# Kernel tuning notes

Measured on AMD Instinct MI355X. Metric: run time of the kernel, lower is better.

## Reference

```python
import jax, jax.numpy as jnp
import numpy as np

B, P, N, M = 8, 50, 128, 128          # batch, pomo, query nodes, route tokens
EMB, H, D = 128, 8, 16                # embedding_dim, head_num, qkv_dim
NE, K = 8, 2                          # num_experts, top-k
CLIP = 10.0                           # logit_clipping


def setup_inputs() -> dict:
    key = jax.random.key(0)
    ks = jax.random.split(key, 12)
    s = 0.02
    return {
        "encoded_nodes": jax.random.normal(ks[0], (B, P, N, EMB), jnp.float32),
        "encoded_routes": jax.random.normal(ks[1], (B, P, M, EMB + 1), jnp.float32),
        "ninf_mask": jnp.zeros((B, P, N), jnp.float32),
        "route_mask": jnp.zeros((B, P, N, M), jnp.float32),
        "Wq": s * jax.random.normal(ks[2], (EMB, H * D), jnp.float32),
        "Wk": s * jax.random.normal(ks[3], (EMB + 1, H * D), jnp.float32),
        "Wv": s * jax.random.normal(ks[4], (EMB + 1, H * D), jnp.float32),
        "Wg": s * jax.random.normal(ks[5], (H * D, NE), jnp.float32),
        "We": s * jax.random.normal(ks[6], (NE, H * D, EMB + 1), jnp.float32),
        "be": jnp.zeros((NE, EMB + 1), jnp.float32),
        "Wfinal": s * jax.random.normal(ks[7], (EMB + 1, 1), jnp.float32),
    }


def _heads(x, W):
    # x: [B,P,n,F] @ W[F,H*D] -> [B,P,H,n,D]
    y = x @ W
    b, p, n, _ = y.shape
    return jnp.swapaxes(y.reshape(b, p, n, H, D), 2, 3)


def reference(encoded_nodes, encoded_routes, ninf_mask, route_mask,
              Wq, Wk, Wv, Wg, We, be, Wfinal):
    # --- masked multi-head attention (multi_head_attention1) ---
    q = _heads(encoded_nodes, Wq)          # [B,P,H,N,D]
    k = _heads(encoded_routes, Wk)         # [B,P,H,M,D]
    v = _heads(encoded_routes, Wv)         # [B,P,H,M,D]
    score = jnp.einsum('bphnd,bphmd->bphnm', q, k) / jnp.sqrt(jnp.float32(D))
    score = score + route_mask[:, :, None, :, :]          # rank3 ninf mask
    w = jax.nn.softmax(score, axis=-1)
    # rank2 mask applied multiplicatively after softmax
    keep = jnp.where(ninf_mask == 0.0, 1.0, 0.0)[:, :, None, :, None]
    w = w * keep
    out = jnp.einsum('bphnm,bphmd->bphnd', w, v)
    out_concat = jnp.swapaxes(out, 2, 3).reshape(B, P, N, H * D)

    # --- top-k gated MoE combine (noisy gating, eval: no noise) ---
    x = out_concat.reshape(-1, H * D)                     # [T, H*D]
    T = x.shape[0]
    gate_logits = x @ Wg                                  # [T, NE]
    top_vals, top_idx = jax.lax.top_k(gate_logits, K)
    top_g = jax.nn.softmax(top_vals, axis=-1)
    gates = jnp.zeros((T, NE), x.dtype).at[jnp.arange(T)[:, None], top_idx].set(top_g)
    expert_out = jnp.einsum('ti,eio->teo', x, We) + be    # [T, NE, EMB+1]
    moe_out = jnp.einsum('te,teo->to', gates, expert_out)
    importance = gates.sum(0)
    moe_loss = importance.var() / (importance.mean() ** 2 + 1e-10)
    mh_atten_out = moe_out.reshape(B, P, N, EMB + 1)

    # --- final scoring ---
    score_scaled = (mh_atten_out @ Wfinal)[..., 0]        # [B,P,N]
    score_clipped = CLIP * jnp.tanh(score_scaled)
    score_masked = score_clipped + ninf_mask
    probs = jax.nn.softmax(score_masked, axis=2)
    return probs, moe_loss
```

## Files before the change

kernel.cpp:

```cpp
#include <hip/hip_runtime.h>

constexpr int B  = 8,  P = 50, N = 128, M = 128;
constexpr int EMB = 128, H = 8, D = 16;
constexpr int NE = 8;
constexpr int HD = H * D;
constexpr int E1 = EMB + 1;
constexpr int BP = B * P;
constexpr int T  = BP * N;

__global__ void prep_kernel(const float* __restrict__ We,
                            const float* __restrict__ be,
                            const float* __restrict__ Wf,
                            float* __restrict__ Wep, float* __restrict__ bpv,
                            float* __restrict__ importance) {
    const int e = blockIdx.x;
    const int f = threadIdx.x;

    float a = 0.f;
    const long base = ((long)e * HD + f) * E1;
    for (int o = 0; o < E1; ++o) a += We[base + o] * Wf[o];
    Wep[e * HD + f] = a;

    if (f == 0) {
        float b = 0.f;
        for (int o = 0; o < E1; ++o) b += be[(long)e * E1 + o] * Wf[o];
        bpv[e] = b;
    }
    if (e == 0 && f < NE) importance[f] = 0.f;
}

__global__ __launch_bounds__(256) void proj_kernel(
    const float* __restrict__ nodes,
    const float* __restrict__ routes,
    const float* __restrict__ Wq, const float* __restrict__ Wk,
    const float* __restrict__ Wv,
    float* __restrict__ qo, float* __restrict__ ko, float* __restrict__ vo) {
    const int mat = blockIdx.y;
    const float* __restrict__ X = (mat == 0) ? nodes : routes;
    const float* __restrict__ W = (mat == 0) ? Wq : (mat == 1 ? Wk : Wv);
    float* __restrict__ out     = (mat == 0) ? qo : (mat == 1 ? ko : vo);
    const int Kd = (mat == 0) ? EMB : E1;
    const int nit = (Kd + 7) >> 3;

    const int row0 = blockIdx.x * 128;
    const int tid  = threadIdx.x;
    const int tr   = tid >> 4;
    const int tc   = tid & 15;

    __shared__ float XT[2][8][132];
    __shared__ float WS[2][8][132];

    float acc[8][8];
    #pragma unroll
    for (int i = 0; i < 8; ++i)
        #pragma unroll
        for (int j = 0; j < 8; ++j) acc[i][j] = 0.f;

    float xr[4];
    float4 wr;
    const int xkx = tid & 7, xrr = tid >> 3;
    const int wkx = tid >> 5, wc4 = (tid & 31) * 4;

    {
        #pragma unroll
        for (int i = 0; i < 4; ++i) {
            int kg = xkx;
            xr[i] = (kg < Kd) ? X[(long)(row0 + xrr + i * 32) * Kd + kg] : 0.f;
        }
        wr = (wkx < Kd) ? *(const float4*)&W[(long)wkx * HD + wc4]
                        : make_float4(0.f, 0.f, 0.f, 0.f);
        #pragma unroll
        for (int i = 0; i < 4; ++i) XT[0][xkx][xrr + i * 32] = xr[i];
        *(float4*)&WS[0][wkx][wc4] = wr;
    }
    __syncthreads();

    for (int it = 0; it < nit; ++it) {
        const int buf = it & 1;
        if (it + 1 < nit) {
            const int kk = (it + 1) * 8;
            #pragma unroll
            for (int i = 0; i < 4; ++i) {
                int kg = kk + xkx;
                xr[i] = (kg < Kd) ? X[(long)(row0 + xrr + i * 32) * Kd + kg] : 0.f;
            }
            int kg = kk + wkx;
            wr = (kg < Kd) ? *(const float4*)&W[(long)kg * HD + wc4]
                           : make_float4(0.f, 0.f, 0.f, 0.f);
        }

        #pragma unroll
        for (int k = 0; k < 8; ++k) {
            float4 xa = *(const float4*)&XT[buf][k][tr * 4];
            float4 xb = *(const float4*)&XT[buf][k][64 + tr * 4];
            float4 wa = *(const float4*)&WS[buf][k][tc * 4];
            float4 wb = *(const float4*)&WS[buf][k][64 + tc * 4];
            float xv[8] = {xa.x, xa.y, xa.z, xa.w, xb.x, xb.y, xb.z, xb.w};
            float wvv[8] = {wa.x, wa.y, wa.z, wa.w, wb.x, wb.y, wb.z, wb.w};
            #pragma unroll
            for (int i = 0; i < 8; ++i)
                #pragma unroll
                for (int j = 0; j < 8; ++j) acc[i][j] += xv[i] * wvv[j];
        }

        if (it + 1 < nit) {
            const int nb = buf ^ 1;
            #pragma unroll
            for (int i = 0; i < 4; ++i) XT[nb][xkx][xrr + i * 32] = xr[i];
            *(float4*)&WS[nb][wkx][wc4] = wr;
        }
        __syncthreads();
    }

    #pragma unroll
    for (int i = 0; i < 8; ++i) {
        int r = row0 + (i < 4 ? 0 : 64) + tr * 4 + (i & 3);
        float4 o0 = make_float4(acc[i][0], acc[i][1], acc[i][2], acc[i][3]);
        float4 o1 = make_float4(acc[i][4], acc[i][5], acc[i][6], acc[i][7]);
        *(float4*)&out[(long)r * HD + tc * 4]      = o0;
        *(float4*)&out[(long)r * HD + 64 + tc * 4] = o1;
    }
}

__global__ __launch_bounds__(64) void attn_kernel(
    const float* __restrict__ qbuf,
    const float* __restrict__ kbuf,
    const float* __restrict__ vbuf,
    const float* __restrict__ rmask,
    const float* __restrict__ ninf,
    float* __restrict__ xcat) {
    const int bp  = blockIdx.x;
    const int h   = blockIdx.y;
    const int tid = threadIdx.x;

    __shared__ float kh[M][D];

    #pragma unroll
    for (int i = 0; i < 8; ++i) {
        int e = tid + i * 64;
        int r = e >> 2, c4 = (e & 3) * 4;
        *(float4*)&kh[r][c4] = *(const float4*)&kbuf[((long)bp * M + r) * HD + h * D + c4];
    }
    __syncthreads();

    const long t0 = (long)bp * N + tid, t1 = t0 + 64;

    float qr0[16], qr1[16];
    {
        const float4* q0 = (const float4*)&qbuf[t0 * HD + h * D];
        const float4* q1 = (const float4*)&qbuf[t1 * HD + h * D];
        #pragma unroll
        for (int i = 0; i < 4; ++i) {
            float4 a = q0[i], b = q1[i];
            qr0[i*4+0] = a.x*0.25f; qr0[i*4+1] = a.y*0.25f;
            qr0[i*4+2] = a.z*0.25f; qr0[i*4+3] = a.w*0.25f;
            qr1[i*4+0] = b.x*0.25f; qr1[i*4+1] = b.y*0.25f;
            qr1[i*4+2] = b.z*0.25f; qr1[i*4+3] = b.w*0.25f;
        }
    }

    const float* __restrict__ vbase = vbuf + ((long)bp * M) * HD + h * D;
    const float4* rm0 = (const float4*)&rmask[t0 * M];
    const float4* rm1 = (const float4*)&rmask[t1 * M];

    float sum0 = 0.f, sum1 = 0.f;
    float o0[16], o1[16];
    #pragma unroll
    for (int d = 0; d < 16; ++d) { o0[d] = 0.f; o1[d] = 0.f; }

    for (int mb = 0; mb < 32; ++mb) {
        float4 r0 = rm0[mb], r1 = rm1[mb];
        float r0v[4] = {r0.x, r0.y, r0.z, r0.w};
        float r1v[4] = {r1.x, r1.y, r1.z, r1.w};
        #pragma unroll
        for (int j = 0; j < 4; ++j) {
            const int m = mb * 4 + j;
            const float4* k4 = (const float4*)&kh[m][0];
            const float4* v4 = (const float4*)&vbase[(long)m * HD];
            float s0 = 0.f, s1 = 0.f;
            #pragma unroll
            for (int q4 = 0; q4 < 4; ++q4) {
                float4 kq = k4[q4];
                s0 += qr0[q4*4+0]*kq.x + qr0[q4*4+1]*kq.y
                    + qr0[q4*4+2]*kq.z + qr0[q4*4+3]*kq.w;
                s1 += qr1[q4*4+0]*kq.x + qr1[q4*4+1]*kq.y
                    + qr1[q4*4+2]*kq.z + qr1[q4*4+3]*kq.w;
            }
            float e0 = __expf(s0 + r0v[j]);
            float e1 = __expf(s1 + r1v[j]);
            sum0 += e0; sum1 += e1;
            #pragma unroll
            for (int q4 = 0; q4 < 4; ++q4) {
                float4 vq = v4[q4];
                o0[q4*4+0] += e0*vq.x; o0[q4*4+1] += e0*vq.y;
                o0[q4*4+2] += e0*vq.z; o0[q4*4+3] += e0*vq.w;
                o1[q4*4+0] += e1*vq.x; o1[q4*4+1] += e1*vq.y;
                o1[q4*4+2] += e1*vq.z; o1[q4*4+3] += e1*vq.w;
            }
        }
    }

    const float inv0 = ((ninf[t0] == 0.f) ? 1.f : 0.f) / sum0;
    const float inv1 = ((ninf[t1] == 0.f) ? 1.f : 0.f) / sum1;
    #pragma unroll
    for (int q4 = 0; q4 < 4; ++q4) {
        float4 w0 = make_float4(o0[q4*4+0]*inv0, o0[q4*4+1]*inv0,
                                o0[q4*4+2]*inv0, o0[q4*4+3]*inv0);
        float4 w1 = make_float4(o1[q4*4+0]*inv1, o1[q4*4+1]*inv1,
                                o1[q4*4+2]*inv1, o1[q4*4+3]*inv1);
        *(float4*)&xcat[t0 * HD + h * D + q4 * 4] = w0;
        *(float4*)&xcat[t1 * HD + h * D + q4 * 4] = w1;
    }
}

__global__ __launch_bounds__(128) void moe_final_kernel(
    const float* __restrict__ xcat, const float* __restrict__ Wg,
    const float* __restrict__ ninf, const float* __restrict__ Wep,
    const float* __restrict__ bpv, float* __restrict__ importance,
    float* __restrict__ out) {
    __shared__ float WgS[EMB][NE];
    __shared__ float WeS[NE][132];
    __shared__ float red[N];
    __shared__ float impS[NE];

    const int bp = blockIdx.x;
    const int n  = threadIdx.x;

    #pragma unroll
    for (int i = 0; i < 2; ++i) {
        int e = n + i * 128;
        int r = e >> 1, c4 = (e & 1) * 4;
        *(float4*)&WgS[r][c4] = *(const float4*)&Wg[(long)r * NE + c4];
    }
    #pragma unroll
    for (int i = 0; i < 2; ++i) {
        int idx = n + i * 128;
        int r = idx >> 5, c = (idx & 31) * 4;
        *(float4*)&WeS[r][c] = *(const float4*)&Wep[(long)r * HD + c];
    }
    if (n < NE) impS[n] = 0.f;
    __syncthreads();

    const long t = (long)bp * N + n;
    const float4* row4 = (const float4*)&xcat[t * HD];

    float gl[NE];
    #pragma unroll
    for (int e = 0; e < NE; ++e) gl[e] = 0.f;
    for (int fb = 0; fb < 32; ++fb) {
        float4 xv = row4[fb];
        float x4[4] = {xv.x, xv.y, xv.z, xv.w};
        #pragma unroll
        for (int j = 0; j < 4; ++j)
            #pragma unroll
            for (int e = 0; e < NE; ++e) gl[e] += x4[j] * WgS[fb * 4 + j][e];
    }

    int e0 = 0; float v0 = gl[0];
    #pragma unroll
    for (int e = 1; e < NE; ++e) if (gl[e] > v0) { v0 = gl[e]; e0 = e; }
    int e1 = -1; float v1 = -3.4e38f;
    #pragma unroll
    for (int e = 0; e < NE; ++e) if (e != e0 && gl[e] > v1) { v1 = gl[e]; e1 = e; }
    float ex = __expf(v1 - v0);
    float g0 = 1.f / (1.f + ex);
    float g1 = ex / (1.f + ex);

    atomicAdd(&impS[e0], g0);
    atomicAdd(&impS[e1], g1);

    float s = g0 * bpv[e0] + g1 * bpv[e1];
    for (int fb = 0; fb < 32; ++fb) {
        float4 xv = row4[fb];
        float x4[4] = {xv.x, xv.y, xv.z, xv.w};
        #pragma unroll
        for (int j = 0; j < 4; ++j) {
            int f = fb * 4 + j;
            s += x4[j] * (g0 * WeS[e0][f] + g1 * WeS[e1][f]);
        }
    }
    s = 10.f * tanhf(s) + ninf[t];

    red[n] = s;
    __syncthreads();
    for (int off = 64; off > 0; off >>= 1) {
        if (n < off) red[n] = fmaxf(red[n], red[n + off]);
        __syncthreads();
    }
    float mx = red[0];
    __syncthreads();
    float e = __expf(s - mx);
    red[n] = e;
    __syncthreads();
    for (int off = 64; off > 0; off >>= 1) {
        if (n < off) red[n] += red[n + off];
        __syncthreads();
    }
    float sum = red[0];

    out[t] = e / sum;

    if (n < NE) atomicAdd(&importance[n], impS[n]);
}

__global__ void loss_kernel(const float* __restrict__ importance,
                            float* __restrict__ out) {
    if (threadIdx.x == 0) {
        float mean = 0.f;
        #pragma unroll
        for (int e = 0; e < NE; ++e) mean += importance[e];
        mean *= (1.f / NE);
        float var = 0.f;
        #pragma unroll
        for (int e = 0; e < NE; ++e) {
            float d = importance[e] - mean;
            var += d * d;
        }
        var *= (1.f / NE);
        out[T] = var / (mean * mean + 1e-10f);
    }
}

extern "C" void kernel_launch(void* const* d_in, const int* in_sizes, int n_in,
                              void* d_out, int out_size, void* d_ws, size_t ws_size,
                              hipStream_t stream) {
    const float* nodes  = (const float*)d_in[0];
    const float* routes = (const float*)d_in[1];
    const float* ninf   = (const float*)d_in[2];
    const float* rmask  = (const float*)d_in[3];
    const float* Wq     = (const float*)d_in[4];
    const float* Wk     = (const float*)d_in[5];
    const float* Wv     = (const float*)d_in[6];
    const float* Wg     = (const float*)d_in[7];
    const float* We     = (const float*)d_in[8];
    const float* be     = (const float*)d_in[9];
    const float* Wfin   = (const float*)d_in[10];

    float* ws = (float*)d_ws;
    float* Wep        = ws + 16;
    float* bpv        = ws + 1040;
    float* importance = ws + 1048;
    float* qbuf       = ws + 4096;
    float* kbuf       = qbuf + (long)T * HD;
    float* vbuf       = kbuf + (long)T * HD;
    float* xcat       = vbuf + (long)T * HD;

    float* out = (float*)d_out;

    prep_kernel<<<NE, 128, 0, stream>>>(We, be, Wfin, Wep, bpv, importance);
    proj_kernel<<<dim3(400, 3), 256, 0, stream>>>(nodes, routes, Wq, Wk, Wv,
                                                  qbuf, kbuf, vbuf);
    attn_kernel<<<dim3(BP, H), 64, 0, stream>>>(qbuf, kbuf, vbuf,
                                                rmask, ninf, xcat);
    moe_final_kernel<<<BP, 128, 0, stream>>>(xcat, Wg, ninf, Wep, bpv,
                                             importance, out);
    loss_kernel<<<1, 64, 0, stream>>>(importance, out);
}
```

Measured before the change: 299.8 us.

## Prefetch route-mask tiles ahead and fold loss into last MoE block via ticket

The attention loop now loads route-mask float4 tiles two iterations ahead, so the global loads overlap with the score and value compute. The separate single-thread loss kernel is removed: each MoE block takes an atomic ticket after adding its importance, and the last block computes the variance-over-mean-squared loss. This saves one kernel launch at the cost of a fence and an atomic per block. It depends on the ticket being reset in prep_kernel on every call.

```diff
diff --git a/kernel.cpp b/kernel.cpp
--- a/kernel.cpp
+++ b/kernel.cpp
@@ -12,7 +12,8 @@
                             const float* __restrict__ be,
                             const float* __restrict__ Wf,
                             float* __restrict__ Wep, float* __restrict__ bpv,
-                            float* __restrict__ importance) {
+                            float* __restrict__ importance,
+                            unsigned* __restrict__ ticket) {
     const int e = blockIdx.x;
     const int f = threadIdx.x;
 
@@ -27,6 +28,7 @@
         bpv[e] = b;
     }
     if (e == 0 && f < NE) importance[f] = 0.f;
+    if (e == 0 && f == NE) *ticket = 0u;
 }
 
 __global__ __launch_bounds__(256) void proj_kernel(
@@ -168,10 +170,14 @@
     #pragma unroll
     for (int d = 0; d < 16; ++d) { o0[d] = 0.f; o1[d] = 0.f; }
 
+    float4 a0 = rm0[0], a1 = rm1[0];
+    float4 b0 = rm0[1], b1 = rm1[1];
+
     for (int mb = 0; mb < 32; ++mb) {
-        float4 r0 = rm0[mb], r1 = rm1[mb];
-        float r0v[4] = {r0.x, r0.y, r0.z, r0.w};
-        float r1v[4] = {r1.x, r1.y, r1.z, r1.w};
+        const int mn = (mb + 2 < 32) ? (mb + 2) : 31;
+        float4 c0 = rm0[mn], c1 = rm1[mn];
+        float r0v[4] = {a0.x, a0.y, a0.z, a0.w};
+        float r1v[4] = {a1.x, a1.y, a1.z, a1.w};
         #pragma unroll
         for (int j = 0; j < 4; ++j) {
             const int m = mb * 4 + j;
@@ -198,6 +204,7 @@
                 o1[q4*4+2] += e1*vq.z; o1[q4*4+3] += e1*vq.w;
             }
         }
+        a0 = b0; a1 = b1; b0 = c0; b1 = c1;
     }
 
     const float inv0 = ((ninf[t0] == 0.f) ? 1.f : 0.f) / sum0;
@@ -217,7 +224,7 @@
     const float* __restrict__ xcat, const float* __restrict__ Wg,
     const float* __restrict__ ninf, const float* __restrict__ Wep,
     const float* __restrict__ bpv, float* __restrict__ importance,
-    float* __restrict__ out) {
+    unsigned* __restrict__ ticket, float* __restrict__ out) {
     __shared__ float WgS[EMB][NE];
     __shared__ float WeS[NE][132];
     __shared__ float red[N];
@@ -301,23 +308,30 @@
     out[t] = e / sum;
 
     if (n < NE) atomicAdd(&importance[n], impS[n]);
-}
-
-__global__ void loss_kernel(const float* __restrict__ importance,
-                            float* __restrict__ out) {
-    if (threadIdx.x == 0) {
-        float mean = 0.f;
-        #pragma unroll
-        for (int e = 0; e < NE; ++e) mean += importance[e];
-        mean *= (1.f / NE);
-        float var = 0.f;
-        #pragma unroll
-        for (int e = 0; e < NE; ++e) {
-            float d = importance[e] - mean;
-            var += d * d;
-        }
-        var *= (1.f / NE);
-        out[T] = var / (mean * mean + 1e-10f);
+
+    __syncthreads();
+    if (n == 0) {
+        __threadfence();
+        unsigned tk = atomicAdd(ticket, 1u);
+        if (tk == BP - 1) {
+            __threadfence();
+            float imp[NE];
+            #pragma unroll
+            for (int ei = 0; ei < NE; ++ei)
+                imp[ei] = atomicAdd(&importance[ei], 0.f);
+            float mean = 0.f;
+            #pragma unroll
+            for (int ei = 0; ei < NE; ++ei) mean += imp[ei];
+            mean *= (1.f / NE);
+            float var = 0.f;
+            #pragma unroll
+            for (int ei = 0; ei < NE; ++ei) {
+                float d = imp[ei] - mean;
+                var += d * d;
+            }
+            var *= (1.f / NE);
+            out[T] = var / (mean * mean + 1e-10f);
+        }
     }
 }
 
@@ -340,6 +354,7 @@
     float* Wep        = ws + 16;
     float* bpv        = ws + 1040;
     float* importance = ws + 1048;
+    unsigned* ticket  = (unsigned*)(ws + 1056);
     float* qbuf       = ws + 4096;
     float* kbuf       = qbuf + (long)T * HD;
     float* vbuf       = kbuf + (long)T * HD;
@@ -347,12 +362,12 @@
 
     float* out = (float*)d_out;
 
-    prep_kernel<<<NE, 128, 0, stream>>>(We, be, Wfin, Wep, bpv, importance);
+    prep_kernel<<<NE, 128, 0, stream>>>(We, be, Wfin, Wep, bpv, importance,
+                                        ticket);
     proj_kernel<<<dim3(400, 3), 256, 0, stream>>>(nodes, routes, Wq, Wk, Wv,
                                                   qbuf, kbuf, vbuf);
     attn_kernel<<<dim3(BP, H), 64, 0, stream>>>(qbuf, kbuf, vbuf,
                                                 rmask, ninf, xcat);
     moe_final_kernel<<<BP, 128, 0, stream>>>(xcat, Wg, ninf, Wep, bpv,
-                                             importance, out);
-    loss_kernel<<<1, 64, 0, stream>>>(importance, out);
-}
+                                             importance, ticket, out);
+}
```

New measurement: 300.6 us. About the same (+0.3%).
